# Optimization experiments

Hardware: AMD Instinct MI355X
Metric: run time of the kernel (lower is better)

Reference implementation:

```python
import jax, jax.numpy as jnp
import numpy as np

D_MODEL = 1024
N_HEADS = 16
D_K = D_MODEL // N_HEADS
B, L = 4, 2048


def setup_inputs() -> dict:
    key = jax.random.key(0)
    ks = jax.random.split(key, 9)
    s = 1.0 / np.sqrt(D_MODEL)
    return {
        "x": jax.random.normal(ks[0], (B, L, D_MODEL), dtype=jnp.float32),
        "mask": jnp.ones((B, L), dtype=jnp.int32),
        "Wq": jax.random.uniform(ks[1], (D_MODEL, D_MODEL), jnp.float32, -s, s),
        "bq": jax.random.uniform(ks[2], (D_MODEL,), jnp.float32, -s, s),
        "Wk": jax.random.uniform(ks[3], (D_MODEL, D_MODEL), jnp.float32, -s, s),
        "bk": jax.random.uniform(ks[4], (D_MODEL,), jnp.float32, -s, s),
        "Wv": jax.random.uniform(ks[5], (D_MODEL, D_MODEL), jnp.float32, -s, s),
        "bv": jax.random.uniform(ks[6], (D_MODEL,), jnp.float32, -s, s),
        "Wo": jax.random.uniform(ks[7], (D_MODEL, D_MODEL), jnp.float32, -s, s),
        "bo": jax.random.uniform(ks[8], (D_MODEL,), jnp.float32, -s, s),
    }


def reference(x, mask, Wq, bq, Wk, bk, Wv, bv, Wo, bo):
    b, l, d = x.shape
    # project and split heads: [B, H, L, d_k]
    def heads(W, bias):
        return (x @ W.T + bias).reshape(b, l, N_HEADS, D_K).transpose(0, 2, 1, 3)
    Q = heads(Wq, bq)
    K = heads(Wk, bk)
    V = heads(Wv, bv)
    scores = jnp.einsum("bhqd,bhkd->bhqk", Q, K) / np.sqrt(D_K).astype(np.float32)
    # mask: [B, L] -> broadcast over heads and query dim as [B, 1, 1, L]
    scores = jnp.where(mask[:, None, None, :] == 0, jnp.float32(-1e9), scores)
    attn = jax.nn.softmax(scores, axis=-1)  # dropout=0 in eval math
    out = jnp.einsum("bhqk,bhkd->bhqd", attn, V)
    out = out.transpose(0, 2, 1, 3).reshape(b, l, d)
    return out @ Wo.T + bo
```

## Files before the change

### kernel.cpp

```cpp
#include <hip/hip_runtime.h>
#include <stdint.h>

#define DMODEL 1024
#define NHEADS 16
#define DK     64
#define BATCH  4
#define SEQ    2048
#define MROWS  (BATCH*SEQ)

typedef __bf16 bf16x8 __attribute__((ext_vector_type(8)));
typedef float  f32x4  __attribute__((ext_vector_type(4)));

#if defined(__has_builtin)
#if __has_builtin(__builtin_amdgcn_exp2f)
#define EXP2F(x) __builtin_amdgcn_exp2f(x)
#endif
#endif
#ifndef EXP2F
#define EXP2F(x) exp2f(x)
#endif

__device__ __forceinline__ unsigned short f2bf(float f) {
    unsigned int u = __builtin_bit_cast(unsigned int, f);
    u += 0x7fffu + ((u >> 16) & 1u);
    return (unsigned short)(u >> 16);
}

__device__ __forceinline__ unsigned int pack_bf16(float a, float b) {
    unsigned int ua = __builtin_bit_cast(unsigned int, a) + 0x8000u;
    unsigned int ub = __builtin_bit_cast(unsigned int, b) + 0x8000u;
    return __builtin_amdgcn_perm(ub, ua, 0x07060302u);
}

#define GLDS(gp, lp) __builtin_amdgcn_global_load_lds( \
    (const __attribute__((address_space(1))) unsigned int*)(gp), \
    (__attribute__((address_space(3))) unsigned int*)(lp), 16, 0, 0)

__global__ void cvt_kernel(const float* __restrict__ src,
                           unsigned short* __restrict__ dst, int n4) {
    int i = blockIdx.x * blockDim.x + threadIdx.x;
    if (i >= n4) return;
    const float4 v = reinterpret_cast<const float4*>(src)[i];
    ushort4 o;
    o.x = f2bf(v.x); o.y = f2bf(v.y); o.z = f2bf(v.z); o.w = f2bf(v.w);
    reinterpret_cast<ushort4*>(dst)[i] = o;
}

__global__ void cvtw_kernel(const float* __restrict__ w0, const float* __restrict__ w1,
                            const float* __restrict__ w2, const float* __restrict__ w3,
                            unsigned short* __restrict__ d0, unsigned short* __restrict__ d1,
                            unsigned short* __restrict__ d2, unsigned short* __restrict__ d3) {
    const float* s; unsigned short* d;
    switch (blockIdx.y) {
        case 0:  s = w0; d = d0; break;
        case 1:  s = w1; d = d1; break;
        case 2:  s = w2; d = d2; break;
        default: s = w3; d = d3; break;
    }
    const int i = blockIdx.x * blockDim.x + threadIdx.x;
    const float4 v = reinterpret_cast<const float4*>(s)[i];
    ushort4 o;
    o.x = f2bf(v.x); o.y = f2bf(v.y); o.z = f2bf(v.z); o.w = f2bf(v.w);
    reinterpret_cast<ushort4*>(d)[i] = o;
}

__global__ void maskbias_kernel(const int* __restrict__ m, float* __restrict__ o, int n) {
    const int i = blockIdx.x * blockDim.x + threadIdx.x;
    if (i < n) o[i] = m[i] ? 0.f : -1e30f;
}

template<int MODE>
__global__ __launch_bounds__(256, 3) void gemm128(
        const unsigned short* __restrict__ A,
        const unsigned short* __restrict__ W0,
        const unsigned short* __restrict__ W1,
        const unsigned short* __restrict__ W2,
        const float* __restrict__ b0,
        const float* __restrict__ b1,
        const float* __restrict__ b2,
        void* __restrict__ o0, void* __restrict__ o1, void* __restrict__ o2) {
    __shared__ unsigned short As[128 * 64];
    __shared__ unsigned short Bs[128 * 64];
    const int lane = threadIdx.x & 63;
    const int wave = threadIdx.x >> 6;
    const int quad = lane >> 4;
    const int r15  = lane & 15;
    const int wr = wave >> 1, wc = wave & 1;
    const int m0 = blockIdx.y * 128;

    int which, ncol0;
    const unsigned short* W;
    const float* bias;
    if (MODE == 0) {
        which = blockIdx.x >> 3;
        ncol0 = (blockIdx.x & 7) * 128;
        W    = which == 0 ? W0 : (which == 1 ? W1 : W2);
        bias = which == 0 ? b0 : (which == 1 ? b1 : b2);
    } else {
        which = 0; ncol0 = blockIdx.x * 128; W = W0; bias = b0;
    }

    const int srow = lane >> 3;
    const int scg  = (lane & 7) ^ srow;
    const unsigned short* Ag[4];
    const unsigned short* Wg[4];
    #pragma unroll
    for (int j = 0; j < 4; ++j) {
        const int row = (wave * 4 + j) * 8 + srow;
        Ag[j] = A + (m0 + row) * DMODEL + scg * 8;
        Wg[j] = W + (ncol0 + row) * DMODEL + scg * 8;
    }

    f32x4 acc[4][4] = {};
    for (int kk = 0; kk < DMODEL; kk += 64) {
        __syncthreads();
        #pragma unroll
        for (int j = 0; j < 4; ++j) {
            GLDS(Ag[j] + kk, &As[(wave * 4 + j) * 512]);
            GLDS(Wg[j] + kk, &Bs[(wave * 4 + j) * 512]);
        }
        __syncthreads();
        #pragma unroll
        for (int u = 0; u < 2; ++u) {
            bf16x8 af[4], bfx[4];
            const int cs = ((u * 4 + quad) ^ (r15 & 7)) * 8;
            #pragma unroll
            for (int t = 0; t < 4; ++t) {
                af[t]  = *(const bf16x8*)&As[(wr * 64 + t * 16 + r15) * 64 + cs];
                bfx[t] = *(const bf16x8*)&Bs[(wc * 64 + t * 16 + r15) * 64 + cs];
            }
            #pragma unroll
            for (int mt = 0; mt < 4; ++mt)
                #pragma unroll
                for (int nt = 0; nt < 4; ++nt)
                    acc[mt][nt] = __builtin_amdgcn_mfma_f32_16x16x32_bf16(
                        af[mt], bfx[nt], acc[mt][nt], 0, 0, 0);
        }
    }

    #pragma unroll
    for (int mt = 0; mt < 4; ++mt) {
        #pragma unroll
        for (int nt = 0; nt < 4; ++nt) {
            #pragma unroll
            for (int r = 0; r < 4; ++r) {
                const int row = m0 + wr * 64 + mt * 16 + quad * 4 + r;
                const int col = ncol0 + wc * 64 + nt * 16 + r15;
                float v = acc[mt][nt][r] + bias[col];
                if (MODE == 1) {
                    ((float*)o0)[(size_t)row * DMODEL + col] = v;
                } else {
                    if (which == 0) v *= 0.18033688011112042f;
                    const int b = row >> 11, l = row & (SEQ - 1);
                    const int h = col >> 6,  d = col & (DK - 1);
                    const int bh = b * NHEADS + h;
                    unsigned short* ow = (unsigned short*)(which == 0 ? o0 : (which == 1 ? o1 : o2));
                    size_t idx;
                    if (which < 2) idx = ((size_t)bh * SEQ + l) * DK + d;
                    else           idx = (size_t)bh * (SEQ * DK) + (l >> 6) * (DK * 64) + d * 64 + (l & 63);
                    ow[idx] = f2bf(v);
                }
            }
        }
    }
}

__global__ __launch_bounds__(256, 3) void flash_attn(
        const unsigned short* __restrict__ Q,
        const unsigned short* __restrict__ Km,
        const unsigned short* __restrict__ Vm,
        const float* __restrict__ mbf,
        unsigned short* __restrict__ Oa) {
    __shared__ unsigned short Ks[2][64 * 64];
    __shared__ unsigned short Vs[2][64 * 64];
    __shared__ unsigned short Pl[4][2][16 * 64];
    const int lane = threadIdx.x & 63;
    const int wave = threadIdx.x >> 6;
    const int quad = lane >> 4;
    const int r15  = lane & 15;

    const int id   = (blockIdx.y << 4) | blockIdx.x;
    const int xcd  = id & 7;
    const int slot = id >> 3;
    const int bh   = xcd + ((slot >> 4) << 3);
    const int qt   = slot & 15;
    const int b = bh >> 4, h = bh & (NHEADS - 1);
    const int q0 = qt * 128 + wave * 32;

    const unsigned short* Qb = Q  + (size_t)bh * SEQ * DK;
    const unsigned short* Kb = Km + (size_t)bh * SEQ * DK;
    const unsigned short* Vb = Vm + (size_t)bh * SEQ * DK;
    const float* mb = mbf + b * SEQ;

    const int srow = lane >> 3;
    const int soff = ((lane >> 3) * 64) + (((lane & 7) ^ srow) * 8);

    bf16x8 bq[2][2];
    #pragma unroll
    for (int qf = 0; qf < 2; ++qf)
        #pragma unroll
        for (int u = 0; u < 2; ++u)
            bq[qf][u] = *(const bf16x8*)(Qb + (q0 + qf * 16 + r15) * DK + u * 32 + quad * 8);

    float l_part[2] = {0.f, 0.f};
    f32x4 oacc[2][4] = {};

    #pragma unroll
    for (int j = 0; j < 2; ++j) {
        const int wseg = wave * 2 + j;
        GLDS(Kb + wseg * 512 + soff, &Ks[0][wseg * 512]);
        GLDS(Vb + wseg * 512 + soff, &Vs[0][wseg * 512]);
    }
    __syncthreads();

    int cur = 0;
    for (int kb = 0; kb < SEQ; kb += 64, cur ^= 1) {
        if (kb + 64 < SEQ) {
            const unsigned short* Kg = Kb + (kb + 64) * 64;
            const unsigned short* Vg = Vb + (kb + 64) * 64;
            #pragma unroll
            for (int j = 0; j < 2; ++j) {
                const int wseg = wave * 2 + j;
                GLDS(Kg + wseg * 512 + soff, &Ks[cur ^ 1][wseg * 512]);
                GLDS(Vg + wseg * 512 + soff, &Vs[cur ^ 1][wseg * 512]);
            }
        }

        char* const Pb = (char*)&Pl[wave][0][0];
        #pragma unroll
        for (int t = 0; t < 4; ++t) {
            const bf16x8 ak0 = *(const bf16x8*)&Ks[cur][(t * 16 + r15) * 64 + ((quad ^ (r15 & 7)) * 8)];
            const bf16x8 ak1 = *(const bf16x8*)&Ks[cur][(t * 16 + r15) * 64 + (((4 + quad) ^ (r15 & 7)) * 8)];
            const float4 m4 = *(const float4*)(mb + kb + t * 16 + quad * 4);
            #pragma unroll
            for (int qf = 0; qf < 2; ++qf) {
                f32x4 z = {};
                z = __builtin_amdgcn_mfma_f32_16x16x32_bf16(ak0, bq[qf][0], z, 0, 0, 0);
                z = __builtin_amdgcn_mfma_f32_16x16x32_bf16(ak1, bq[qf][1], z, 0, 0, 0);
                const float p0 = EXP2F(z[0] + m4.x);
                const float p1 = EXP2F(z[1] + m4.y);
                const float p2 = EXP2F(z[2] + m4.z);
                const float p3 = EXP2F(z[3] + m4.w);
                l_part[qf] += (p0 + p1) + (p2 + p3);
                uint2 pw;
                pw.x = pack_bf16(p0, p1);
                pw.y = pack_bf16(p2, p3);
                const int c2 = (t * 2 + (quad >> 1)) ^ (r15 & 7);
                *(uint2*)(Pb + qf * 2048 + r15 * 128 + c2 * 16 + (quad & 1) * 8) = pw;
            }
        }
        asm volatile("s_waitcnt lgkmcnt(0)" ::: "memory");

        #pragma unroll
        for (int u = 0; u < 2; ++u) {
            const int cs = ((u * 4 + quad) ^ (r15 & 7)) * 8;
            bf16x8 vf[4];
            #pragma unroll
            for (int nt = 0; nt < 4; ++nt)
                vf[nt] = *(const bf16x8*)&Vs[cur][(nt * 16 + r15) * 64 + cs];
            #pragma unroll
            for (int qf = 0; qf < 2; ++qf) {
                const bf16x8 ap = *(const bf16x8*)(Pb + qf * 2048 + r15 * 128 + cs * 2);
                #pragma unroll
                for (int nt = 0; nt < 4; ++nt)
                    oacc[qf][nt] = __builtin_amdgcn_mfma_f32_16x16x32_bf16(
                        ap, vf[nt], oacc[qf][nt], 0, 0, 0);
            }
        }

        __syncthreads();
    }

    #pragma unroll
    for (int qf = 0; qf < 2; ++qf) {
        float l = l_part[qf];
        l += __shfl_xor(l, 16);
        l += __shfl_xor(l, 32);
        float lq[4];
        #pragma unroll
        for (int r = 0; r < 4; ++r) lq[r] = __shfl(l, quad * 4 + r, 64);
        #pragma unroll
        for (int nt = 0; nt < 4; ++nt) {
            #pragma unroll
            for (int r = 0; r < 4; ++r) {
                const int row = q0 + qf * 16 + quad * 4 + r;
                const int col = h * DK + nt * 16 + r15;
                Oa[((size_t)b * SEQ + row) * DMODEL + col] = f2bf(oacc[qf][nt][r] / lq[r]);
            }
        }
    }
}

extern "C" void kernel_launch(void* const* d_in, const int* in_sizes, int n_in,
                              void* d_out, int out_size, void* d_ws, size_t ws_size,
                              hipStream_t stream) {
    (void)in_sizes; (void)n_in; (void)out_size; (void)ws_size;
    const float* x  = (const float*)d_in[0];
    const int* mask = (const int*)d_in[1];
    const float* Wq = (const float*)d_in[2];
    const float* bq = (const float*)d_in[3];
    const float* Wk = (const float*)d_in[4];
    const float* bk = (const float*)d_in[5];
    const float* Wv = (const float*)d_in[6];
    const float* bv = (const float*)d_in[7];
    const float* Wo = (const float*)d_in[8];
    const float* bo = (const float*)d_in[9];
    float* out = (float*)d_out;

    char* ws = (char*)d_ws;
    unsigned short* xb  = (unsigned short*)(ws);
    unsigned short* wqb = (unsigned short*)(ws + 16777216);
    unsigned short* wkb = (unsigned short*)(ws + 16777216 + 1 * 2097152);
    unsigned short* wvb = (unsigned short*)(ws + 16777216 + 2 * 2097152);
    unsigned short* wob = (unsigned short*)(ws + 16777216 + 3 * 2097152);
    unsigned short* qb  = (unsigned short*)(ws + 16777216 + 4 * 2097152);
    unsigned short* kb  = qb  + (size_t)MROWS * DMODEL;
    unsigned short* vtb = kb  + (size_t)MROWS * DMODEL;
    unsigned short* ab  = vtb + (size_t)MROWS * DMODEL;
    float*          mbf = (float*)(ab + (size_t)MROWS * DMODEL);

    cvt_kernel<<<dim3(MROWS * DMODEL / 4 / 256), 256, 0, stream>>>(x, xb, MROWS * DMODEL / 4);
    cvtw_kernel<<<dim3(DMODEL * DMODEL / 4 / 256, 4), 256, 0, stream>>>(
        Wq, Wk, Wv, Wo, wqb, wkb, wvb, wob);
    maskbias_kernel<<<dim3(BATCH * SEQ / 256), 256, 0, stream>>>(mask, mbf, BATCH * SEQ);

    gemm128<0><<<dim3(24, MROWS / 128), 256, 0, stream>>>(
        xb, wqb, wkb, wvb, bq, bk, bv, qb, kb, vtb);

    flash_attn<<<dim3(16, BATCH * NHEADS), 256, 0, stream>>>(qb, kb, vtb, mbf, ab);

    gemm128<1><<<dim3(8, MROWS / 128), 256, 0, stream>>>(
        ab, wob, nullptr, nullptr, bo, nullptr, nullptr, out, nullptr, nullptr);
}
```

Before: 325.7 us.

## Single-buffer V tile in flash attention to fit four blocks per CU

The V shared-memory tile goes from double to single buffering, and launch bounds rise from 3 to 4 blocks per SM. The next V tile is now loaded after the P·V step, and an extra block barrier between the QK/softmax phase and P·V makes sure the load has landed. The per-tile mask loads are also hoisted into registers at the top of each iteration. The aim is to cut LDS use so more waves stay resident and hide latency better. The cost is an extra barrier per tile and V load latency that is only covered by the QK compute, plus tighter register limits.

```diff
diff --git a/kernel.cpp b/kernel.cpp
--- a/kernel.cpp
+++ b/kernel.cpp
@@ -165,14 +165,14 @@
     }
 }
 
-__global__ __launch_bounds__(256, 3) void flash_attn(
+__global__ __launch_bounds__(256, 4) void flash_attn(
         const unsigned short* __restrict__ Q,
         const unsigned short* __restrict__ Km,
         const unsigned short* __restrict__ Vm,
         const float* __restrict__ mbf,
         unsigned short* __restrict__ Oa) {
     __shared__ unsigned short Ks[2][64 * 64];
-    __shared__ unsigned short Vs[2][64 * 64];
+    __shared__ unsigned short Vs[64 * 64];
     __shared__ unsigned short Pl[4][2][16 * 64];
     const int lane = threadIdx.x & 63;
     const int wave = threadIdx.x >> 6;
@@ -209,29 +209,35 @@
     for (int j = 0; j < 2; ++j) {
         const int wseg = wave * 2 + j;
         GLDS(Kb + wseg * 512 + soff, &Ks[0][wseg * 512]);
-        GLDS(Vb + wseg * 512 + soff, &Vs[0][wseg * 512]);
+        GLDS(Vb + wseg * 512 + soff, &Vs[wseg * 512]);
     }
     __syncthreads();
 
-    int cur = 0;
-    for (int kb = 0; kb < SEQ; kb += 64, cur ^= 1) {
-        if (kb + 64 < SEQ) {
+    #define NT (SEQ / 64)
+    for (int t = 0; t < NT; ++t) {
+        const int kb = t * 64;
+        const int cur = t & 1;
+
+        float4 m4v[4];
+        #pragma unroll
+        for (int tt = 0; tt < 4; ++tt)
+            m4v[tt] = *(const float4*)(mb + kb + tt * 16 + quad * 4);
+
+        if (t + 1 < NT) {
             const unsigned short* Kg = Kb + (kb + 64) * 64;
-            const unsigned short* Vg = Vb + (kb + 64) * 64;
             #pragma unroll
             for (int j = 0; j < 2; ++j) {
                 const int wseg = wave * 2 + j;
                 GLDS(Kg + wseg * 512 + soff, &Ks[cur ^ 1][wseg * 512]);
-                GLDS(Vg + wseg * 512 + soff, &Vs[cur ^ 1][wseg * 512]);
             }
         }
 
         char* const Pb = (char*)&Pl[wave][0][0];
         #pragma unroll
-        for (int t = 0; t < 4; ++t) {
-            const bf16x8 ak0 = *(const bf16x8*)&Ks[cur][(t * 16 + r15) * 64 + ((quad ^ (r15 & 7)) * 8)];
-            const bf16x8 ak1 = *(const bf16x8*)&Ks[cur][(t * 16 + r15) * 64 + (((4 + quad) ^ (r15 & 7)) * 8)];
-            const float4 m4 = *(const float4*)(mb + kb + t * 16 + quad * 4);
+        for (int tt = 0; tt < 4; ++tt) {
+            const bf16x8 ak0 = *(const bf16x8*)&Ks[cur][(tt * 16 + r15) * 64 + ((quad ^ (r15 & 7)) * 8)];
+            const bf16x8 ak1 = *(const bf16x8*)&Ks[cur][(tt * 16 + r15) * 64 + (((4 + quad) ^ (r15 & 7)) * 8)];
+            const float4 m4 = m4v[tt];
             #pragma unroll
             for (int qf = 0; qf < 2; ++qf) {
                 f32x4 z = {};
@@ -245,11 +251,12 @@
                 uint2 pw;
                 pw.x = pack_bf16(p0, p1);
                 pw.y = pack_bf16(p2, p3);
-                const int c2 = (t * 2 + (quad >> 1)) ^ (r15 & 7);
+                const int c2 = (tt * 2 + (quad >> 1)) ^ (r15 & 7);
                 *(uint2*)(Pb + qf * 2048 + r15 * 128 + c2 * 16 + (quad & 1) * 8) = pw;
             }
         }
-        asm volatile("s_waitcnt lgkmcnt(0)" ::: "memory");
+
+        __syncthreads();
 
         #pragma unroll
         for (int u = 0; u < 2; ++u) {
@@ -257,7 +264,7 @@
             bf16x8 vf[4];
             #pragma unroll
             for (int nt = 0; nt < 4; ++nt)
-                vf[nt] = *(const bf16x8*)&Vs[cur][(nt * 16 + r15) * 64 + cs];
+                vf[nt] = *(const bf16x8*)&Vs[(nt * 16 + r15) * 64 + cs];
             #pragma unroll
             for (int qf = 0; qf < 2; ++qf) {
                 const bf16x8 ap = *(const bf16x8*)(Pb + qf * 2048 + r15 * 128 + cs * 2);
@@ -269,7 +276,17 @@
         }
 
         __syncthreads();
-    }
+
+        if (t + 1 < NT) {
+            const unsigned short* Vg = Vb + (kb + 64) * 64;
+            #pragma unroll
+            for (int j = 0; j < 2; ++j) {
+                const int wseg = wave * 2 + j;
+                GLDS(Vg + wseg * 512 + soff, &Vs[wseg * 512]);
+            }
+        }
+    }
+    #undef NT
 
     #pragma unroll
     for (int qf = 0; qf < 2; ++qf) {
```

After: 312.5 us. 4.1% less time.

## Rewrite flash attention inner loop with 32x32 MFMA and register-resident P

Applied to the files above, without the earlier changes.

The attention kernel switches from 16x16x32 to 32x32x16 bf16 MFMAs with S computed as K·Q^T. P is converted with v_cvt_pk_bf16_f32 and rearranged across half-waves with shuffles into the A-operand layout, replacing the per-wave LDS staging buffer and its waitcnt. The mask is loaded once into LDS, s_setprio wraps the MFMA sections, and launch bounds rise to 4 blocks per CU. This cuts LDS traffic and MFMA instruction count in exchange for extra shuffles and register pressure that could spill at the higher occupancy target.

```diff
diff --git a/kernel.cpp b/kernel.cpp
--- a/kernel.cpp
+++ b/kernel.cpp
@@ -10,6 +10,7 @@
 
 typedef __bf16 bf16x8 __attribute__((ext_vector_type(8)));
 typedef float  f32x4  __attribute__((ext_vector_type(4)));
+typedef float  f32x16 __attribute__((ext_vector_type(16)));
 
 #if defined(__has_builtin)
 #if __has_builtin(__builtin_amdgcn_exp2f)
@@ -26,10 +27,10 @@
     return (unsigned short)(u >> 16);
 }
 
-__device__ __forceinline__ unsigned int pack_bf16(float a, float b) {
-    unsigned int ua = __builtin_bit_cast(unsigned int, a) + 0x8000u;
-    unsigned int ub = __builtin_bit_cast(unsigned int, b) + 0x8000u;
-    return __builtin_amdgcn_perm(ub, ua, 0x07060302u);
+__device__ __forceinline__ unsigned int cvtpk(float lo, float hi) {
+    unsigned int r;
+    asm("v_cvt_pk_bf16_f32 %0, %1, %2" : "=v"(r) : "v"(lo), "v"(hi));
+    return r;
 }
 
 #define GLDS(gp, lp) __builtin_amdgcn_global_load_lds( \
@@ -165,7 +166,7 @@
     }
 }
 
-__global__ __launch_bounds__(256, 3) void flash_attn(
+__global__ __launch_bounds__(256, 4) void flash_attn(
         const unsigned short* __restrict__ Q,
         const unsigned short* __restrict__ Km,
         const unsigned short* __restrict__ Vm,
@@ -173,18 +174,18 @@
         unsigned short* __restrict__ Oa) {
     __shared__ unsigned short Ks[2][64 * 64];
     __shared__ unsigned short Vs[2][64 * 64];
-    __shared__ unsigned short Pl[4][2][16 * 64];
+    __shared__ float maskl[SEQ];
     const int lane = threadIdx.x & 63;
     const int wave = threadIdx.x >> 6;
-    const int quad = lane >> 4;
-    const int r15  = lane & 15;
+    const int q31  = lane & 31;
+    const int h    = lane >> 5;
 
     const int id   = (blockIdx.y << 4) | blockIdx.x;
     const int xcd  = id & 7;
     const int slot = id >> 3;
     const int bh   = xcd + ((slot >> 4) << 3);
     const int qt   = slot & 15;
-    const int b = bh >> 4, h = bh & (NHEADS - 1);
+    const int b = bh >> 4, hd = bh & (NHEADS - 1);
     const int q0 = qt * 128 + wave * 32;
 
     const unsigned short* Qb = Q  + (size_t)bh * SEQ * DK;
@@ -193,18 +194,16 @@
     const float* mb = mbf + b * SEQ;
 
     const int srow = lane >> 3;
-    const int soff = ((lane >> 3) * 64) + (((lane & 7) ^ srow) * 8);
-
-    bf16x8 bq[2][2];
-    #pragma unroll
-    for (int qf = 0; qf < 2; ++qf)
-        #pragma unroll
-        for (int u = 0; u < 2; ++u)
-            bq[qf][u] = *(const bf16x8*)(Qb + (q0 + qf * 16 + r15) * DK + u * 32 + quad * 8);
-
-    float l_part[2] = {0.f, 0.f};
-    f32x4 oacc[2][4] = {};
-
+    const int soff = srow * 64 + (((lane & 7) ^ srow) * 8);
+
+    bf16x8 bq[4];
+    #pragma unroll
+    for (int s = 0; s < 4; ++s)
+        bq[s] = *(const bf16x8*)(Qb + (q0 + q31) * DK + s * 16 + h * 8);
+
+    #pragma unroll
+    for (int j = 0; j < 2; ++j)
+        GLDS(mb + j * 1024 + wave * 256 + lane * 4, &maskl[j * 1024 + wave * 256]);
     #pragma unroll
     for (int j = 0; j < 2; ++j) {
         const int wseg = wave * 2 + j;
@@ -213,9 +212,14 @@
     }
     __syncthreads();
 
-    int cur = 0;
-    for (int kb = 0; kb < SEQ; kb += 64, cur ^= 1) {
-        if (kb + 64 < SEQ) {
+    f32x16 oacc0 = {}, oacc1 = {};
+    float l_part = 0.f;
+
+    for (int t = 0; t < SEQ / 64; ++t) {
+        const int kb = t * 64;
+        const int cur = t & 1;
+
+        if (t + 1 < SEQ / 64) {
             const unsigned short* Kg = Kb + (kb + 64) * 64;
             const unsigned short* Vg = Vb + (kb + 64) * 64;
             #pragma unroll
@@ -226,68 +230,73 @@
             }
         }
 
-        char* const Pb = (char*)&Pl[wave][0][0];
-        #pragma unroll
-        for (int t = 0; t < 4; ++t) {
-            const bf16x8 ak0 = *(const bf16x8*)&Ks[cur][(t * 16 + r15) * 64 + ((quad ^ (r15 & 7)) * 8)];
-            const bf16x8 ak1 = *(const bf16x8*)&Ks[cur][(t * 16 + r15) * 64 + (((4 + quad) ^ (r15 & 7)) * 8)];
-            const float4 m4 = *(const float4*)(mb + kb + t * 16 + quad * 4);
-            #pragma unroll
-            for (int qf = 0; qf < 2; ++qf) {
-                f32x4 z = {};
-                z = __builtin_amdgcn_mfma_f32_16x16x32_bf16(ak0, bq[qf][0], z, 0, 0, 0);
-                z = __builtin_amdgcn_mfma_f32_16x16x32_bf16(ak1, bq[qf][1], z, 0, 0, 0);
-                const float p0 = EXP2F(z[0] + m4.x);
-                const float p1 = EXP2F(z[1] + m4.y);
-                const float p2 = EXP2F(z[2] + m4.z);
-                const float p3 = EXP2F(z[3] + m4.w);
-                l_part[qf] += (p0 + p1) + (p2 + p3);
-                uint2 pw;
-                pw.x = pack_bf16(p0, p1);
-                pw.y = pack_bf16(p2, p3);
-                const int c2 = (t * 2 + (quad >> 1)) ^ (r15 & 7);
-                *(uint2*)(Pb + qf * 2048 + r15 * 128 + c2 * 16 + (quad & 1) * 8) = pw;
-            }
-        }
-        asm volatile("s_waitcnt lgkmcnt(0)" ::: "memory");
-
-        #pragma unroll
-        for (int u = 0; u < 2; ++u) {
-            const int cs = ((u * 4 + quad) ^ (r15 & 7)) * 8;
-            bf16x8 vf[4];
-            #pragma unroll
-            for (int nt = 0; nt < 4; ++nt)
-                vf[nt] = *(const bf16x8*)&Vs[cur][(nt * 16 + r15) * 64 + cs];
-            #pragma unroll
-            for (int qf = 0; qf < 2; ++qf) {
-                const bf16x8 ap = *(const bf16x8*)(Pb + qf * 2048 + r15 * 128 + cs * 2);
-                #pragma unroll
-                for (int nt = 0; nt < 4; ++nt)
-                    oacc[qf][nt] = __builtin_amdgcn_mfma_f32_16x16x32_bf16(
-                        ap, vf[nt], oacc[qf][nt], 0, 0, 0);
-            }
-        }
+        bf16x8 pa[4];
+        #pragma unroll
+        for (int kt = 0; kt < 2; ++kt) {
+            const int krow = kt * 32 + q31;
+            f32x16 z = {};
+            __builtin_amdgcn_s_setprio(1);
+            #pragma unroll
+            for (int s = 0; s < 4; ++s) {
+                const bf16x8 ak = *(const bf16x8*)&Ks[cur][krow * 64 + (((2 * s + h) ^ (krow & 7)) * 8)];
+                z = __builtin_amdgcn_mfma_f32_32x32x16_bf16(ak, bq[s], z, 0, 0, 0);
+            }
+            __builtin_amdgcn_s_setprio(0);
+
+            float pg[4][4];
+            #pragma unroll
+            for (int g = 0; g < 4; ++g) {
+                const float4 m4 = *(const float4*)&maskl[kb + kt * 32 + g * 8 + h * 4];
+                pg[g][0] = EXP2F(z[4 * g + 0] + m4.x);
+                pg[g][1] = EXP2F(z[4 * g + 1] + m4.y);
+                pg[g][2] = EXP2F(z[4 * g + 2] + m4.z);
+                pg[g][3] = EXP2F(z[4 * g + 3] + m4.w);
+                l_part += (pg[g][0] + pg[g][1]) + (pg[g][2] + pg[g][3]);
+            }
+
+            #pragma unroll
+            for (int hf = 0; hf < 2; ++hf) {
+                const unsigned int Aw = cvtpk(pg[2 * hf][0],     pg[2 * hf][1]);
+                const unsigned int Bw = cvtpk(pg[2 * hf][2],     pg[2 * hf][3]);
+                const unsigned int Cw = cvtpk(pg[2 * hf + 1][0], pg[2 * hf + 1][1]);
+                const unsigned int Dw = cvtpk(pg[2 * hf + 1][2], pg[2 * hf + 1][3]);
+                const unsigned int Asw = (unsigned int)__shfl_xor((int)Aw, 32);
+                const unsigned int Bsw = (unsigned int)__shfl_xor((int)Bw, 32);
+                const unsigned int Csw = (unsigned int)__shfl_xor((int)Cw, 32);
+                const unsigned int Dsw = (unsigned int)__shfl_xor((int)Dw, 32);
+                uint4 w;
+                w.x = h ? Csw : Aw;
+                w.y = h ? Dsw : Bw;
+                w.z = h ? Cw  : Asw;
+                w.w = h ? Dw  : Bsw;
+                pa[2 * kt + hf] = __builtin_bit_cast(bf16x8, w);
+            }
+        }
+
+        __builtin_amdgcn_s_setprio(1);
+        #pragma unroll
+        for (int s = 0; s < 4; ++s) {
+            const int r0 = q31;
+            const int r1 = 32 + q31;
+            const bf16x8 vf0 = *(const bf16x8*)&Vs[cur][r0 * 64 + (((2 * s + h) ^ (r0 & 7)) * 8)];
+            const bf16x8 vf1 = *(const bf16x8*)&Vs[cur][r1 * 64 + (((2 * s + h) ^ (r1 & 7)) * 8)];
+            oacc0 = __builtin_amdgcn_mfma_f32_32x32x16_bf16(pa[s], vf0, oacc0, 0, 0, 0);
+            oacc1 = __builtin_amdgcn_mfma_f32_32x32x16_bf16(pa[s], vf1, oacc1, 0, 0, 0);
+        }
+        __builtin_amdgcn_s_setprio(0);
 
         __syncthreads();
     }
 
-    #pragma unroll
-    for (int qf = 0; qf < 2; ++qf) {
-        float l = l_part[qf];
-        l += __shfl_xor(l, 16);
-        l += __shfl_xor(l, 32);
-        float lq[4];
-        #pragma unroll
-        for (int r = 0; r < 4; ++r) lq[r] = __shfl(l, quad * 4 + r, 64);
-        #pragma unroll
-        for (int nt = 0; nt < 4; ++nt) {
-            #pragma unroll
-            for (int r = 0; r < 4; ++r) {
-                const int row = q0 + qf * 16 + quad * 4 + r;
-                const int col = h * DK + nt * 16 + r15;
-                Oa[((size_t)b * SEQ + row) * DMODEL + col] = f2bf(oacc[qf][nt][r] / lq[r]);
-            }
-        }
+    const float l = l_part + __shfl_xor(l_part, 32);
+    #pragma unroll
+    for (int r = 0; r < 16; ++r) {
+        const int qloc = (r & 3) + 8 * (r >> 2) + 4 * h;
+        const float lq = __shfl(l, qloc);
+        const int row = q0 + qloc;
+        const size_t base = ((size_t)b * SEQ + row) * DMODEL + hd * DK;
+        Oa[base + q31]      = f2bf(oacc0[r] / lq);
+        Oa[base + 32 + q31] = f2bf(oacc1[r] / lq);
     }
 }
 
```

Measured after the change: 319.0 us. -2.0%, faster.
